# Optimization experiments

Hardware: AMD Instinct MI355X
Metric: run time of the kernel (lower is better)

Reference implementation:

```python
import jax, jax.numpy as jnp
import numpy as np

SIZES = [512, 2048, 4096, 8192, 16384]
BATCH = 64
MASK_DENSITY = 0.05  # GO DAG edge masks are very sparse


def setup_inputs() -> dict:
    key = jax.random.key(0)
    keys = jax.random.split(key, 1 + 3 * 4)
    inp = {"x": jax.random.normal(keys[0], (BATCH, SIZES[0]), dtype=jnp.float32)}
    for i in range(4):
        fan_in, fan_out = SIZES[i], SIZES[i + 1]
        scale = 1.0 / np.sqrt(fan_in)
        inp[f"W{i}"] = jax.random.normal(keys[1 + 3 * i], (fan_out, fan_in), dtype=jnp.float32) * scale
        inp[f"b{i}"] = jax.random.normal(keys[2 + 3 * i], (fan_out,), dtype=jnp.float32) * scale
        inp[f"mask{i}"] = jax.random.uniform(keys[3 + 3 * i], (fan_out, fan_in)) < MASK_DENSITY
    return inp


def reference(x, W0, W1, W2, W3, b0, b1, b2, b3, mask0, mask1, mask2, mask3):
    Ws = [W0, W1, W2, W3]
    bs = [b0, b1, b2, b3]
    masks = [mask0, mask1, mask2, mask3]
    n = len(Ws)
    for i in range(n):
        # SparseLinear: weight zeroed outside the GO parent-child edge mask
        Wm = Ws[i] * masks[i].astype(x.dtype)  # [out, in]
        x = x @ Wm.T + bs[i]                   # [B, out]
        if i < n - 1:
            x = jax.nn.relu(x)  # ReLU between all but the last layer
    return x
```

## Files before the change

### kernel.cpp

```cpp
#include <hip/hip_runtime.h>
#include <hip/hip_cooperative_groups.h>
#include <stdint.h>

namespace cg = cooperative_groups;


typedef short bf16x8 __attribute__((ext_vector_type(8)));
typedef float f32x4  __attribute__((ext_vector_type(4)));

__device__ __forceinline__ unsigned short f2bf(float f) {
    unsigned int u = __float_as_uint(f);
    return (unsigned short)((u + 0x7FFFu + ((u >> 16) & 1u)) >> 16);
}

__device__ __forceinline__ unsigned int bfpair(float lo, float hi) {
    return (unsigned int)f2bf(lo) | ((unsigned int)f2bf(hi) << 16);
}

__device__ __forceinline__ bf16x8 pack8(const float4& a, const float4& b) {
    union { unsigned int u[4]; bf16x8 v; } r;
    r.u[0] = bfpair(a.x, a.y);
    r.u[1] = bfpair(a.z, a.w);
    r.u[2] = bfpair(b.x, b.y);
    r.u[3] = bfpair(b.z, b.w);
    return r.v;
}

template <int MU8, int RELU>
__device__ __forceinline__ void gemm_loop(
    const float* __restrict__ X, const float* __restrict__ W,
    const unsigned char* __restrict__ Mk,
    int K, int kbeg, int kend, int n0, int lr, int quad, f32x4 (&acc)[4][4])
{
    const int* __restrict__ Mk32 = (const int*)Mk;
    const size_t xoff = (size_t)lr * K + quad * 8;
    const size_t woff = (size_t)(n0 + lr) * K + quad * 8;

    #pragma unroll 1
    for (int k = kbeg; k < kend; k += 32) {
        bf16x8 bfr[4];
        #pragma unroll
        for (int bg = 0; bg < 4; ++bg) {
            const float* xp = X + xoff + (size_t)bg * 16 * K + k;
            float4 x0 = *(const float4*)xp;
            float4 x1 = *(const float4*)(xp + 4);
            if (RELU) {
                x0.x = fmaxf(x0.x, 0.f); x0.y = fmaxf(x0.y, 0.f);
                x0.z = fmaxf(x0.z, 0.f); x0.w = fmaxf(x0.w, 0.f);
                x1.x = fmaxf(x1.x, 0.f); x1.y = fmaxf(x1.y, 0.f);
                x1.z = fmaxf(x1.z, 0.f); x1.w = fmaxf(x1.w, 0.f);
            }
            bfr[bg] = pack8(x0, x1);
        }
        #pragma unroll
        for (int ng = 0; ng < 4; ++ng) {
            size_t e = woff + (size_t)ng * 16 * K + k;
            float4 w0 = *(const float4*)(W + e);
            float4 w1 = *(const float4*)(W + e + 4);
            if (MU8) {
                uint2 m8 = *(const uint2*)(Mk + e);
                w0.x = (m8.x & 0x000000FFu) ? w0.x : 0.f;
                w0.y = (m8.x & 0x0000FF00u) ? w0.y : 0.f;
                w0.z = (m8.x & 0x00FF0000u) ? w0.z : 0.f;
                w0.w = (m8.x & 0xFF000000u) ? w0.w : 0.f;
                w1.x = (m8.y & 0x000000FFu) ? w1.x : 0.f;
                w1.y = (m8.y & 0x0000FF00u) ? w1.y : 0.f;
                w1.z = (m8.y & 0x00FF0000u) ? w1.z : 0.f;
                w1.w = (m8.y & 0xFF000000u) ? w1.w : 0.f;
            } else {
                int4 mm0 = *(const int4*)(Mk32 + e);
                int4 mm1 = *(const int4*)(Mk32 + e + 4);
                w0.x = mm0.x ? w0.x : 0.f;
                w0.y = mm0.y ? w0.y : 0.f;
                w0.z = mm0.z ? w0.z : 0.f;
                w0.w = mm0.w ? w0.w : 0.f;
                w1.x = mm1.x ? w1.x : 0.f;
                w1.y = mm1.y ? w1.y : 0.f;
                w1.z = mm1.z ? w1.z : 0.f;
                w1.w = mm1.w ? w1.w : 0.f;
            }
            bf16x8 a = pack8(w0, w1);
            #pragma unroll
            for (int bg = 0; bg < 4; ++bg)
                acc[ng][bg] = __builtin_amdgcn_mfma_f32_16x16x32_bf16(
                    a, bfr[bg], acc[ng][bg], 0, 0, 0);
        }
    }
}

template <int MU8, int RELU>
__device__ __forceinline__ void gemm_tile(
    const float* __restrict__ X, const float* __restrict__ W,
    const unsigned char* __restrict__ Mk,
    float* __restrict__ Z, int N, int K,
    int kbeg, int kend, int n0, int lr, int quad)
{
    f32x4 acc[4][4];
    #pragma unroll
    for (int i = 0; i < 4; ++i)
        #pragma unroll
        for (int j = 0; j < 4; ++j) acc[i][j] = (f32x4){0.f, 0.f, 0.f, 0.f};

    gemm_loop<MU8, RELU>(X, W, Mk, K, kbeg, kend, n0, lr, quad, acc);

    #pragma unroll
    for (int ng = 0; ng < 4; ++ng) {
        #pragma unroll
        for (int bg = 0; bg < 4; ++bg) {
            int b = bg * 16 + lr;
            float* zp = Z + (size_t)b * N + n0 + ng * 16 + quad * 4;
            #pragma unroll
            for (int r = 0; r < 4; ++r) atomicAdd(&zp[r], acc[ng][bg][r]);
        }
    }
}

template <int RELU>
__device__ __forceinline__ void run_layer(
    const float* __restrict__ X, const float* __restrict__ W,
    const unsigned char* __restrict__ Mk, int mu8,
    float* __restrict__ Z, int N, int K, int nk,
    int wid, int nw, int lr, int quad)
{
    const int ntx    = N >> 6;
    const int sh     = 31 - __clz(ntx);
    const int kper   = K / nk;
    const int ntiles = ntx * nk;
    for (int t = wid; t < ntiles; t += nw) {
        int n0   = (t & (ntx - 1)) << 6;
        int kbeg = (t >> sh) * kper;
        if (mu8) gemm_tile<1, RELU>(X, W, Mk, Z, N, K, kbeg, kbeg + kper, n0, lr, quad);
        else     gemm_tile<0, RELU>(X, W, Mk, Z, N, K, kbeg, kbeg + kper, n0, lr, quad);
    }
}

__global__ __launch_bounds__(256, 2) void fused_mlp(
    const float* __restrict__ x,
    const float* __restrict__ W0, const float* __restrict__ b0, const unsigned char* __restrict__ m0,
    const float* __restrict__ W1, const float* __restrict__ b1, const unsigned char* __restrict__ m1,
    const float* __restrict__ W2, const float* __restrict__ b2, const unsigned char* __restrict__ m2,
    const float* __restrict__ W3, const float* __restrict__ b3, const unsigned char* __restrict__ m3,
    float* __restrict__ z0, float* __restrict__ z1,
    float* __restrict__ z2, float* __restrict__ z3,
    int nk0, int nk1, int nk2, int nk3)
{
    cg::grid_group grid = cg::this_grid();

    __shared__ int s_any;
    if (threadIdx.x == 0) s_any = 0;
    __syncthreads();
    {
        const unsigned int* mm = (const unsigned int*)m0;
        int any = 0;
        #pragma unroll
        for (int it = 0; it < 16; ++it) {
            unsigned int v = mm[it * 256 + threadIdx.x];
            if (v & 0xFFFFFF00u) any = 1;
        }
        if (__any(any) && (threadIdx.x & 63) == 0) s_any = 1;
    }
    __syncthreads();
    const int mu8 = s_any;

    {
        const unsigned tr = blockIdx.x * 256u + threadIdx.x;
        const unsigned tn = gridDim.x * 256u;
        for (unsigned i = tr; i < 64u * 2048u;  i += tn) z0[i] = b0[i & 2047u];
        for (unsigned i = tr; i < 64u * 4096u;  i += tn) z1[i] = b1[i & 4095u];
        for (unsigned i = tr; i < 64u * 8192u;  i += tn) z2[i] = b2[i & 8191u];
        for (unsigned i = tr; i < 64u * 16384u; i += tn) z3[i] = b3[i & 16383u];
    }

    grid.sync();

    const int wid  = (blockIdx.x << 2) | (threadIdx.x >> 6);
    const int nw   = gridDim.x << 2;
    const int l    = threadIdx.x & 63;
    const int lr   = l & 15;
    const int quad = l >> 4;

    run_layer<0>(x,  W0, m0, mu8, z0, 2048,  512,  nk0, wid, nw, lr, quad);
    grid.sync();
    run_layer<1>(z0, W1, m1, mu8, z1, 4096,  2048, nk1, wid, nw, lr, quad);
    grid.sync();
    run_layer<1>(z1, W2, m2, mu8, z2, 8192,  4096, nk2, wid, nw, lr, quad);
    grid.sync();
    run_layer<1>(z2, W3, m3, mu8, z3, 16384, 8192, nk3, wid, nw, lr, quad);
}


__global__ __launch_bounds__(256) void probe_mask_kind(
    const unsigned int* __restrict__ m, int* __restrict__ flag)
{
    __shared__ int s_any;
    if (threadIdx.x == 0) s_any = 0;
    __syncthreads();
    int any = 0;
    #pragma unroll
    for (int it = 0; it < 16; ++it) {
        unsigned int v = m[it * 256 + threadIdx.x];
        if (v & 0xFFFFFF00u) any = 1;
    }
    if (__any(any) && (threadIdx.x & 63) == 0) s_any = 1;
    __syncthreads();
    if (threadIdx.x == 0) flag[0] = s_any;
}

__global__ __launch_bounds__(256) void init_bias_all(
    const float* __restrict__ b0, const float* __restrict__ b1,
    const float* __restrict__ b2, const float* __restrict__ b3,
    float* __restrict__ z0, float* __restrict__ z1,
    float* __restrict__ z2, float* __restrict__ z3)
{
    int n = blockIdx.x * 256 + threadIdx.x;
    int b = blockIdx.y;
    if (n < 2048)             z0[(size_t)b * 2048  + n]           = b0[n];
    else if (n < 6144)        z1[(size_t)b * 4096  + (n - 2048)]  = b1[n - 2048];
    else if (n < 14336)       z2[(size_t)b * 8192  + (n - 6144)]  = b2[n - 6144];
    else                      z3[(size_t)b * 16384 + (n - 14336)] = b3[n - 14336];
}

__global__ __launch_bounds__(64, 2) void sparse_gemm_rf(
    const float* __restrict__ X, const float* __restrict__ W,
    const unsigned char* __restrict__ Mk, const int* __restrict__ mflag,
    float* __restrict__ Z, int N, int K, int kper, int relu_in)
{
    const int l    = threadIdx.x;
    const int lr   = l & 15;
    const int quad = l >> 4;
    const int n0   = blockIdx.x * 64;
    const int kbeg = blockIdx.y * kper;
    const int mu8  = *mflag;

    if (mu8) {
        if (relu_in) gemm_tile<1, 1>(X, W, Mk, Z, N, K, kbeg, kbeg + kper, n0, lr, quad);
        else         gemm_tile<1, 0>(X, W, Mk, Z, N, K, kbeg, kbeg + kper, n0, lr, quad);
    } else {
        if (relu_in) gemm_tile<0, 1>(X, W, Mk, Z, N, K, kbeg, kbeg + kper, n0, lr, quad);
        else         gemm_tile<0, 0>(X, W, Mk, Z, N, K, kbeg, kbeg + kper, n0, lr, quad);
    }
}

extern "C" void kernel_launch(void* const* d_in, const int* in_sizes, int n_in,
                              void* d_out, int out_size, void* d_ws, size_t ws_size,
                              hipStream_t stream) {
    const float* x  = (const float*)d_in[0];
    const float* W0 = (const float*)d_in[1];
    const float* b0 = (const float*)d_in[2];
    const unsigned char* m0 = (const unsigned char*)d_in[3];
    const float* W1 = (const float*)d_in[4];
    const float* b1 = (const float*)d_in[5];
    const unsigned char* m1 = (const unsigned char*)d_in[6];
    const float* W2 = (const float*)d_in[7];
    const float* b2 = (const float*)d_in[8];
    const unsigned char* m2 = (const unsigned char*)d_in[9];
    const float* W3 = (const float*)d_in[10];
    const float* b3 = (const float*)d_in[11];
    const unsigned char* m3 = (const unsigned char*)d_in[12];

    float* z0 = (float*)d_ws;
    float* z1 = z0 + (size_t)64 * 2048;
    float* z2 = z1 + (size_t)64 * 4096;
    float* z3 = (float*)d_out;

    static int blocksPerCU = -1;
    if (blocksPerCU < 0) {
        hipError_t e = hipOccupancyMaxActiveBlocksPerMultiprocessor(
            &blocksPerCU, reinterpret_cast<const void*>(&fused_mlp), 256, 0);
        if (e != hipSuccess || blocksPerCU <= 0) blocksPerCU = 2;
        if (blocksPerCU > 8) blocksPerCU = 8;
    }
    int G = blocksPerCU * 256;
    if (G > 2048) G = 2048;
    const int WV = G * 4;

    auto pick_nk = [&](int ntx, int K) {
        int nk = 1;
        while (ntx * nk < WV && (K / (nk * 2)) >= 64) nk <<= 1;
        return nk;
    };
    int nk0 = pick_nk(32,  512);
    int nk1 = pick_nk(64,  2048);
    int nk2 = pick_nk(128, 4096);
    int nk3 = pick_nk(256, 8192);

    void* args[] = {
        (void*)&x,
        (void*)&W0, (void*)&b0, (void*)&m0,
        (void*)&W1, (void*)&b1, (void*)&m1,
        (void*)&W2, (void*)&b2, (void*)&m2,
        (void*)&W3, (void*)&b3, (void*)&m3,
        (void*)&z0, (void*)&z1, (void*)&z2, (void*)&z3,
        (void*)&nk0, (void*)&nk1, (void*)&nk2, (void*)&nk3
    };
    hipError_t le = hipLaunchCooperativeKernel(
        reinterpret_cast<const void*>(&fused_mlp),
        dim3(G), dim3(256), args, 0, stream);

    if (le != hipSuccess) {
        int* mflag = (int*)(z2 + (size_t)64 * 8192);
        probe_mask_kind<<<1, 256, 0, stream>>>((const unsigned int*)m0, mflag);
        init_bias_all<<<dim3(120, 64), 256, 0, stream>>>(b0, b1, b2, b3, z0, z1, z2, z3);
        sparse_gemm_rf<<<dim3(32, 8),  64, 0, stream>>>(x,  W0, m0, mflag, z0, 2048,  512,   64, 0);
        sparse_gemm_rf<<<dim3(64, 8),  64, 0, stream>>>(z0, W1, m1, mflag, z1, 4096,  2048, 256, 1);
        sparse_gemm_rf<<<dim3(128, 8), 64, 0, stream>>>(z1, W2, m2, mflag, z2, 8192,  4096, 512, 1);
        sparse_gemm_rf<<<dim3(256, 8), 64, 0, stream>>>(z2, W3, m3, mflag, z3, 16384, 8192, 1024, 1);
    }
}
```

Before: 1.610 ms.

## Stage weight and mask tiles into LDS with async double-buffered global_load_lds

```diff
diff --git a/kernel.cpp b/kernel.cpp
--- a/kernel.cpp
+++ b/kernel.cpp
@@ -26,8 +26,123 @@
     return r.v;
 }
 
+__device__ __forceinline__ void gll16(const void* src, void* dst) {
+    __builtin_amdgcn_global_load_lds(
+        (const __attribute__((address_space(1))) unsigned int*)src,
+        (__attribute__((address_space(3))) unsigned int*)dst, 16, 0, 0);
+}
+
+__device__ __forceinline__ void stage_chunk(
+    const float* wsrc, const int* msrc, int K, float* lw, int* lm)
+{
+    #pragma unroll
+    for (int i = 0; i < 8; ++i) {
+        gll16(wsrc + (size_t)i * 8 * K, lw + i * 256);
+        gll16(msrc + (size_t)i * 8 * K, lm + i * 256);
+    }
+}
+
+template <int RELU>
+__device__ __forceinline__ void gemm_tile_lds(
+    const float* __restrict__ X, const float* __restrict__ W,
+    const int* __restrict__ M, float* __restrict__ Z,
+    int N, int K, int kbeg, int kper, int n0,
+    int l, int lr, int q, float* lwb, int* lmb)
+{
+    const int nc  = kper >> 5;
+    const int rr  = l >> 3;
+    const int gl4 = (((l & 7) ^ (rr & 7)) << 2);
+
+    f32x4 acc[4][4];
+    #pragma unroll
+    for (int i = 0; i < 4; ++i)
+        #pragma unroll
+        for (int j = 0; j < 4; ++j) acc[i][j] = (f32x4){0.f, 0.f, 0.f, 0.f};
+
+    const float* wsrc0 = W + (size_t)(n0 + rr) * K + kbeg + gl4;
+    const int*   msrc0 = M + (size_t)(n0 + rr) * K + kbeg + gl4;
+    const float* xb    = X + (size_t)lr * K + q * 8;
+
+    stage_chunk(wsrc0, msrc0, K, lwb, lmb);
+
+    #pragma unroll 1
+    for (int c = 0; c < nc; ++c) {
+        const int p  = c & 1;
+        const int kk = kbeg + c * 32;
+
+        float4 xv0[4], xv1[4];
+        #pragma unroll
+        for (int bg = 0; bg < 4; ++bg) {
+            const float* xp = xb + kk + (size_t)bg * 16 * K;
+            xv0[bg] = *(const float4*)xp;
+            xv1[bg] = *(const float4*)(xp + 4);
+        }
+
+        if (c + 1 < nc) {
+            stage_chunk(wsrc0 + (c + 1) * 32, msrc0 + (c + 1) * 32, K,
+                        lwb + (p ^ 1) * 2048, lmb + (p ^ 1) * 2048);
+            asm volatile("s_waitcnt vmcnt(16)" ::: "memory");
+        } else {
+            asm volatile("s_waitcnt vmcnt(0)" ::: "memory");
+        }
+
+        bf16x8 bfr[4];
+        #pragma unroll
+        for (int bg = 0; bg < 4; ++bg) {
+            float4 x0 = xv0[bg], x1 = xv1[bg];
+            if (RELU) {
+                x0.x = fmaxf(x0.x, 0.f); x0.y = fmaxf(x0.y, 0.f);
+                x0.z = fmaxf(x0.z, 0.f); x0.w = fmaxf(x0.w, 0.f);
+                x1.x = fmaxf(x1.x, 0.f); x1.y = fmaxf(x1.y, 0.f);
+                x1.z = fmaxf(x1.z, 0.f); x1.w = fmaxf(x1.w, 0.f);
+            }
+            bfr[bg] = pack8(x0, x1);
+        }
+
+        const float* lw = lwb + p * 2048;
+        const int*   lm = lmb + p * 2048;
+        const int s  = lr & 7;
+        const int p0 = (((2 * q)     ^ s) << 2);
+        const int p1 = (((2 * q + 1) ^ s) << 2);
+        #pragma unroll
+        for (int ng = 0; ng < 4; ++ng) {
+            const int R = ng * 16 + lr;
+            const float* wr = lw + R * 32;
+            const int*   mr = lm + R * 32;
+            float4 w0 = *(const float4*)(wr + p0);
+            float4 w1 = *(const float4*)(wr + p1);
+            int4  mm0 = *(const int4*)(mr + p0);
+            int4  mm1 = *(const int4*)(mr + p1);
+            w0.x = mm0.x ? w0.x : 0.f;
+            w0.y = mm0.y ? w0.y : 0.f;
+            w0.z = mm0.z ? w0.z : 0.f;
+            w0.w = mm0.w ? w0.w : 0.f;
+            w1.x = mm1.x ? w1.x : 0.f;
+            w1.y = mm1.y ? w1.y : 0.f;
+            w1.z = mm1.z ? w1.z : 0.f;
+            w1.w = mm1.w ? w1.w : 0.f;
+            bf16x8 a = pack8(w0, w1);
+            #pragma unroll
+            for (int bg = 0; bg < 4; ++bg)
+                acc[ng][bg] = __builtin_amdgcn_mfma_f32_16x16x32_bf16(
+                    a, bfr[bg], acc[ng][bg], 0, 0, 0);
+        }
+    }
+
+    #pragma unroll
+    for (int ng = 0; ng < 4; ++ng) {
+        #pragma unroll
+        for (int bg = 0; bg < 4; ++bg) {
+            int b = bg * 16 + lr;
+            float* zp = Z + (size_t)b * N + n0 + ng * 16 + q * 4;
+            #pragma unroll
+            for (int r = 0; r < 4; ++r) atomicAdd(&zp[r], acc[ng][bg][r]);
+        }
+    }
+}
+
 template <int MU8, int RELU>
-__device__ __forceinline__ void gemm_loop(
+__device__ __forceinline__ void gemm_loop_reg(
     const float* __restrict__ X, const float* __restrict__ W,
     const unsigned char* __restrict__ Mk,
     int K, int kbeg, int kend, int n0, int lr, int quad, f32x4 (&acc)[4][4])
@@ -89,7 +204,7 @@
 }
 
 template <int MU8, int RELU>
-__device__ __forceinline__ void gemm_tile(
+__device__ __forceinline__ void gemm_tile_reg(
     const float* __restrict__ X, const float* __restrict__ W,
     const unsigned char* __restrict__ Mk,
     float* __restrict__ Z, int N, int K,
@@ -101,7 +216,7 @@
         #pragma unroll
         for (int j = 0; j < 4; ++j) acc[i][j] = (f32x4){0.f, 0.f, 0.f, 0.f};
 
-    gemm_loop<MU8, RELU>(X, W, Mk, K, kbeg, kend, n0, lr, quad, acc);
+    gemm_loop_reg<MU8, RELU>(X, W, Mk, K, kbeg, kend, n0, lr, quad, acc);
 
     #pragma unroll
     for (int ng = 0; ng < 4; ++ng) {
@@ -119,52 +234,51 @@
 __device__ __forceinline__ void run_layer(
     const float* __restrict__ X, const float* __restrict__ W,
     const unsigned char* __restrict__ Mk, int mu8,
-    float* __restrict__ Z, int N, int K, int nk,
-    int wid, int nw, int lr, int quad)
+    float* __restrict__ Z, int N, int K, int nk, int kper,
+    int wid, int nw, int l, int lr, int quad, float* lwb, int* lmb)
 {
     const int ntx    = N >> 6;
     const int sh     = 31 - __clz(ntx);
-    const int kper   = K / nk;
     const int ntiles = ntx * nk;
     for (int t = wid; t < ntiles; t += nw) {
         int n0   = (t & (ntx - 1)) << 6;
         int kbeg = (t >> sh) * kper;
-        if (mu8) gemm_tile<1, RELU>(X, W, Mk, Z, N, K, kbeg, kbeg + kper, n0, lr, quad);
-        else     gemm_tile<0, RELU>(X, W, Mk, Z, N, K, kbeg, kbeg + kper, n0, lr, quad);
-    }
-}
-
-__global__ __launch_bounds__(256, 2) void fused_mlp(
+        if (mu8)
+            gemm_tile_reg<1, RELU>(X, W, Mk, Z, N, K, kbeg, kbeg + kper, n0, lr, quad);
+        else
+            gemm_tile_lds<RELU>(X, W, (const int*)Mk, Z, N, K, kbeg, kper, n0,
+                                l, lr, quad, lwb, lmb);
+    }
+}
+
+__global__ __launch_bounds__(64, 2) void fused_mlp(
     const float* __restrict__ x,
     const float* __restrict__ W0, const float* __restrict__ b0, const unsigned char* __restrict__ m0,
     const float* __restrict__ W1, const float* __restrict__ b1, const unsigned char* __restrict__ m1,
     const float* __restrict__ W2, const float* __restrict__ b2, const unsigned char* __restrict__ m2,
     const float* __restrict__ W3, const float* __restrict__ b3, const unsigned char* __restrict__ m3,
     float* __restrict__ z0, float* __restrict__ z1,
-    float* __restrict__ z2, float* __restrict__ z3,
-    int nk0, int nk1, int nk2, int nk3)
+    float* __restrict__ z2, float* __restrict__ z3)
 {
     cg::grid_group grid = cg::this_grid();
 
-    __shared__ int s_any;
-    if (threadIdx.x == 0) s_any = 0;
-    __syncthreads();
+    __shared__ float lwbuf[2][2048];
+    __shared__ int   lmbuf[2][2048];
+
+    int any = 0;
     {
         const unsigned int* mm = (const unsigned int*)m0;
-        int any = 0;
         #pragma unroll
         for (int it = 0; it < 16; ++it) {
-            unsigned int v = mm[it * 256 + threadIdx.x];
+            unsigned int v = mm[it * 64 + threadIdx.x];
             if (v & 0xFFFFFF00u) any = 1;
         }
-        if (__any(any) && (threadIdx.x & 63) == 0) s_any = 1;
-    }
-    __syncthreads();
-    const int mu8 = s_any;
+    }
+    const int mu8 = (__any(any) ? 1 : 0);
 
     {
-        const unsigned tr = blockIdx.x * 256u + threadIdx.x;
-        const unsigned tn = gridDim.x * 256u;
+        const unsigned tr = blockIdx.x * 64u + threadIdx.x;
+        const unsigned tn = gridDim.x * 64u;
         for (unsigned i = tr; i < 64u * 2048u;  i += tn) z0[i] = b0[i & 2047u];
         for (unsigned i = tr; i < 64u * 4096u;  i += tn) z1[i] = b1[i & 4095u];
         for (unsigned i = tr; i < 64u * 8192u;  i += tn) z2[i] = b2[i & 8191u];
@@ -173,19 +287,21 @@
 
     grid.sync();
 
-    const int wid  = (blockIdx.x << 2) | (threadIdx.x >> 6);
-    const int nw   = gridDim.x << 2;
-    const int l    = threadIdx.x & 63;
+    const int wid  = blockIdx.x;
+    const int nw   = gridDim.x;
+    const int l    = threadIdx.x;
     const int lr   = l & 15;
     const int quad = l >> 4;
-
-    run_layer<0>(x,  W0, m0, mu8, z0, 2048,  512,  nk0, wid, nw, lr, quad);
+    float* lwb = &lwbuf[0][0];
+    int*   lmb = &lmbuf[0][0];
+
+    run_layer<0>(x,  W0, m0, mu8, z0, 2048,  512,   8,   64, wid, nw, l, lr, quad, lwb, lmb);
     grid.sync();
-    run_layer<1>(z0, W1, m1, mu8, z1, 4096,  2048, nk1, wid, nw, lr, quad);
+    run_layer<1>(z0, W1, m1, mu8, z1, 4096,  2048, 16,  128, wid, nw, l, lr, quad, lwb, lmb);
     grid.sync();
-    run_layer<1>(z1, W2, m2, mu8, z2, 8192,  4096, nk2, wid, nw, lr, quad);
+    run_layer<1>(z1, W2, m2, mu8, z2, 8192,  4096,  8,  512, wid, nw, l, lr, quad, lwb, lmb);
     grid.sync();
-    run_layer<1>(z2, W3, m3, mu8, z3, 16384, 8192, nk3, wid, nw, lr, quad);
+    run_layer<1>(z2, W3, m3, mu8, z3, 16384, 8192,  4, 2048, wid, nw, l, lr, quad, lwb, lmb);
 }
 
 
@@ -233,11 +349,11 @@
     const int mu8  = *mflag;
 
     if (mu8) {
-        if (relu_in) gemm_tile<1, 1>(X, W, Mk, Z, N, K, kbeg, kbeg + kper, n0, lr, quad);
-        else         gemm_tile<1, 0>(X, W, Mk, Z, N, K, kbeg, kbeg + kper, n0, lr, quad);
+        if (relu_in) gemm_tile_reg<1, 1>(X, W, Mk, Z, N, K, kbeg, kbeg + kper, n0, lr, quad);
+        else         gemm_tile_reg<1, 0>(X, W, Mk, Z, N, K, kbeg, kbeg + kper, n0, lr, quad);
     } else {
-        if (relu_in) gemm_tile<0, 1>(X, W, Mk, Z, N, K, kbeg, kbeg + kper, n0, lr, quad);
-        else         gemm_tile<0, 0>(X, W, Mk, Z, N, K, kbeg, kbeg + kper, n0, lr, quad);
+        if (relu_in) gemm_tile_reg<0, 1>(X, W, Mk, Z, N, K, kbeg, kbeg + kper, n0, lr, quad);
+        else         gemm_tile_reg<0, 0>(X, W, Mk, Z, N, K, kbeg, kbeg + kper, n0, lr, quad);
     }
 }
 
@@ -266,23 +382,11 @@
     static int blocksPerCU = -1;
     if (blocksPerCU < 0) {
         hipError_t e = hipOccupancyMaxActiveBlocksPerMultiprocessor(
-            &blocksPerCU, reinterpret_cast<const void*>(&fused_mlp), 256, 0);
-        if (e != hipSuccess || blocksPerCU <= 0) blocksPerCU = 2;
-        if (blocksPerCU > 8) blocksPerCU = 8;
+            &blocksPerCU, reinterpret_cast<const void*>(&fused_mlp), 64, 0);
+        if (e != hipSuccess || blocksPerCU <= 0) blocksPerCU = 4;
     }
     int G = blocksPerCU * 256;
-    if (G > 2048) G = 2048;
-    const int WV = G * 4;
-
-    auto pick_nk = [&](int ntx, int K) {
-        int nk = 1;
-        while (ntx * nk < WV && (K / (nk * 2)) >= 64) nk <<= 1;
-        return nk;
-    };
-    int nk0 = pick_nk(32,  512);
-    int nk1 = pick_nk(64,  2048);
-    int nk2 = pick_nk(128, 4096);
-    int nk3 = pick_nk(256, 8192);
+    if (G > 1024) G = 1024;
 
     void* args[] = {
         (void*)&x,
@@ -290,12 +394,11 @@
         (void*)&W1, (void*)&b1, (void*)&m1,
         (void*)&W2, (void*)&b2, (void*)&m2,
         (void*)&W3, (void*)&b3, (void*)&m3,
-        (void*)&z0, (void*)&z1, (void*)&z2, (void*)&z3,
-        (void*)&nk0, (void*)&nk1, (void*)&nk2, (void*)&nk3
+        (void*)&z0, (void*)&z1, (void*)&z2, (void*)&z3
     };
     hipError_t le = hipLaunchCooperativeKernel(
         reinterpret_cast<const void*>(&fused_mlp),
-        dim3(G), dim3(256), args, 0, stream);
+        dim3(G), dim3(64), args, 0, stream);
 
     if (le != hipSuccess) {
         int* mflag = (int*)(z2 + (size_t)64 * 8192);
```

Measured after the change: 1.748 ms. 8.5% more time.
